# Performance work log

Hardware: AMD Instinct MI355X
Metric: run time of the kernel (lower is better)

Reference implementation:

```python
import jax, jax.numpy as jnp
import numpy as np

B, S, V, D, F, NC = 256, 64, 100000, 64, 10, 10  # batch, seq, vocab, emb_dim, n_feats, n_clusters


def setup_inputs() -> dict:
    key = jax.random.key(0)
    ks = jax.random.split(key, 12)
    ids = jax.random.randint(ks[0], (B, S), 0, V)
    emb_table = jax.random.normal(ks[1], (V, D), dtype=jnp.float32) * 0.02
    comb_w1 = jax.random.normal(ks[2], (2 * D, D), dtype=jnp.float32) / np.sqrt(2 * D)
    comb_b1 = jnp.zeros((D,), jnp.float32)
    comb_w2 = jax.random.normal(ks[3], (D, F), dtype=jnp.float32) / np.sqrt(D)
    comb_b2 = jnp.zeros((F,), jnp.float32)
    freq_w1 = jax.random.normal(ks[4], (D + 1, D), dtype=jnp.float32) / np.sqrt(D + 1)
    freq_b1 = jnp.zeros((D,), jnp.float32)
    freq_w2 = jax.random.normal(ks[5], (D, F), dtype=jnp.float32) / np.sqrt(D)
    freq_b2 = jnp.zeros((F,), jnp.float32)
    cluster_centers = jax.random.normal(ks[6], (NC, D), dtype=jnp.float32)
    cat_freq = jnp.ones((V,), jnp.float32)          # category_frequencies buffer
    total_samples = jnp.array(1.0, jnp.float32)     # total_samples buffer
    return dict(category_ids=ids, emb_table=emb_table,
                comb_w1=comb_w1, comb_b1=comb_b1, comb_w2=comb_w2, comb_b2=comb_b2,
                freq_w1=freq_w1, freq_b1=freq_b1, freq_w2=freq_w2, freq_b2=freq_b2,
                cluster_centers=cluster_centers, cat_freq=cat_freq,
                total_samples=total_samples)


def reference(category_ids, emb_table, comb_w1, comb_b1, comb_w2, comb_b2,
              freq_w1, freq_b1, freq_w2, freq_b2, cluster_centers,
              cat_freq, total_samples):
    emb = emb_table[category_ids]                      # [B,S,D]
    # --- pairwise combination features (vectorized over all i<j pairs) ---
    iu, ju = np.triu_indices(S, 1)                     # P = S*(S-1)/2 pairs
    P = iu.shape[0]
    pairs = jnp.concatenate([emb[:, iu], emb[:, ju]], axis=-1)   # [B,P,2D]
    h = jax.nn.relu(jnp.einsum('bpe,ed->bpd', pairs, comb_w1) + comb_b1)
    combo = jnp.einsum('bpd,df->bpf', h, comb_w2) + comb_b2      # [B,P,F]
    combo_sum = combo.sum(axis=1)                      # [B,F]
    # --- frequency features ---
    freqs = cat_freq[category_ids] / total_samples     # [B,S]
    freq_in = jnp.concatenate([emb, freqs[..., None]], axis=-1)  # [B,S,D+1]
    fh = jax.nn.relu(jnp.einsum('bse,ed->bsd', freq_in, freq_w1) + freq_b1)
    freq_feat = jnp.einsum('bsd,df->bsf', fh, freq_w2) + freq_b2  # [B,S,F]
    # --- cluster assignment features (softmax over -euclidean distances) ---
    d2 = (jnp.sum(emb * emb, axis=-1, keepdims=True)
          + jnp.sum(cluster_centers * cluster_centers, axis=-1)
          - 2.0 * jnp.einsum('bsd,cd->bsc', emb, cluster_centers))
    dist = jnp.sqrt(jnp.maximum(d2, 0.0))              # [B,S,NC]
    cluster_feat = jax.nn.softmax(-dist, axis=-1)      # [B,S,F] (F==NC)
    # --- mean over stacked features: freq + P pair feats (broadcast over seq) + cluster ---
    out = (freq_feat + combo_sum[:, None, :] + cluster_feat) / (P + 2)
    return out
```

## Files before the change

### kernel.cpp

```cpp
#include <hip/hip_runtime.h>
#include <math.h>


typedef _Float16 h2 __attribute__((ext_vector_type(2)));
typedef _Float16 h4 __attribute__((ext_vector_type(4)));
typedef _Float16 h8 __attribute__((ext_vector_type(8)));
union H4u { h4 v; h2 h[2]; };
union H8u { h8 v; h2 h[4]; };

constexpr int BATCH = 256;
constexpr int S = 64, D = 64, F = 10;
constexpr int NPAIR = S * (S - 1) / 2;

constexpr int EMBS = 6144;
constexpr int U2B  = 8448;
constexpr int V2T  = 10496;
constexpr int FHT  = 12608;
constexpr int DI_F = 14784;
constexpr int W2P  = 15488;
constexpr int FRQ  = 15808;
constexpr int PART_F = 0;

__device__ __forceinline__ h2 pk2(float a, float b) {
#if __has_builtin(__builtin_amdgcn_cvt_pkrtz)
  auto t = __builtin_amdgcn_cvt_pkrtz(a, b);
  return __builtin_bit_cast(h2, t);
#else
  h2 r; r.x = (_Float16)a; r.y = (_Float16)b; return r;
#endif
}

__device__ __forceinline__ float fdot2f(h2 a, h2 b, float c) {
#if __has_builtin(__builtin_amdgcn_fdot2)
  typedef __fp16 q2 __attribute__((ext_vector_type(2)));
  return __builtin_amdgcn_fdot2(__builtin_bit_cast(q2, a),
                                __builtin_bit_cast(q2, b), c, false);
#else
  return c + (float)a.x * (float)b.x + (float)a.y * (float)b.y;
#endif
}

__device__ __forceinline__ h2 hmax2z(h2 a) {
#if __has_builtin(__builtin_elementwise_max)
  h2 z = {(_Float16)0, (_Float16)0};
  return __builtin_elementwise_max(a, z);
#else
  h2 r;
  r.x = a.x > (_Float16)0 ? a.x : (_Float16)0;
  r.y = a.y > (_Float16)0 ? a.y : (_Float16)0;
  return r;
#endif
}

__device__ __forceinline__ float lane_up1(float v) {
#if __has_builtin(__builtin_amdgcn_update_dpp)
  int r = __builtin_amdgcn_update_dpp(0, __float_as_int(v), 0xF5, 0xF, 0xF, false);
  return __int_as_float(r);
#else
  return __shfl_down(v, 1, 64);
#endif
}

__global__ __launch_bounds__(1024, 4)
void cat_enc_kernel(const int*   __restrict__ ids,
                    const float* __restrict__ emb_table,
                    const float* __restrict__ comb_w1,
                    const float* __restrict__ comb_b1,
                    const float* __restrict__ comb_w2,
                    const float* __restrict__ comb_b2,
                    const float* __restrict__ freq_w1,
                    const float* __restrict__ freq_b1,
                    const float* __restrict__ freq_w2,
                    const float* __restrict__ freq_b2,
                    const float* __restrict__ centers,
                    const float* __restrict__ cat_freq,
                    const float* __restrict__ total_samples,
                    float*       __restrict__ out)
{
  __shared__ __align__(16) unsigned int ldsu[15872];
  h2*    ldsH = (h2*)ldsu;
  float* ldsf = (float*)ldsu;
  const int tid = threadIdx.x;
  const int b = blockIdx.x, bBase = b * S;
  float ffreg = 0.f;

  {
    int s = tid >> 4, q = tid & 15;
    int id = ids[bBase + s];
    float4 e4 = *(const float4*)(emb_table + (size_t)id * D + q * 4);
    H4u ep; ep.h[0] = pk2(e4.x, e4.y); ep.h[1] = pk2(e4.z, e4.w);
    *(h4*)&ldsH[EMBS + s * 36 + q * 2] = ep.v;
    if (q == 0) ldsf[FRQ + s] = cat_freq[id];

    {
      const int k4 = tid >> 6, dd = tid & 63;
      const float* s0p = comb_w1 + (k4 * 4) * D + dd;
      const float* s1p = s0p + D * D;
      const float* s2p = freq_w1 + (k4 * 4) * D + dd;
      h4* dst = (h4*)ldsu;
      H4u u0; u0.h[0] = pk2(s0p[0], s0p[D]); u0.h[1] = pk2(s0p[2 * D], s0p[3 * D]);
      H4u u1; u1.h[0] = pk2(s1p[0], s1p[D]); u1.h[1] = pk2(s1p[2 * D], s1p[3 * D]);
      H4u u2; u2.h[0] = pk2(s2p[0], s2p[D]); u2.h[1] = pk2(s2p[2 * D], s2p[3 * D]);
      dst[2 * tid]     = u0.v;
      dst[2 * tid + 1] = u1.v;
      dst[2048 + tid]  = u2.v;
    }
    if (tid < 320) {
      int f = tid >> 5, d2 = tid & 31;
      ldsH[W2P + tid] = pk2(freq_w2[(2 * d2) * F + f], freq_w2[(2 * d2 + 1) * F + f]);
    }
  }
  __syncthreads();

  {
    const int wv   = __builtin_amdgcn_readfirstlane((int)(tid >> 6));
    const int lane = tid & 63;
    if (wv < 8) {
      const int d  = lane;
      const int s0 = wv * 8;
      const float invT = 1.0f / total_samples[0];
      const float b1d = comb_b1[d], fb1d = freq_b1[d], fw1L = freq_w1[D * D + d];
      float aU[8], aV[8], aF[8];
#pragma unroll
      for (int si = 0; si < 8; ++si) {
        aU[si] = b1d; aV[si] = 0.f;
        aF[si] = fmaf(ldsf[FRQ + s0 + si] * invT, fw1L, fb1d);
      }
      const h8* WUVp = (const h8*)ldsu;
      const h4* WFp  = (const h4*)(ldsu + 4096);
#pragma unroll 2
      for (int k8 = 0; k8 < 8; ++k8) {
        H8u wa; wa.v = WUVp[(2 * k8) * 64 + d];
        H8u wb; wb.v = WUVp[(2 * k8 + 1) * 64 + d];
        H4u fa; fa.v = WFp[(2 * k8) * 64 + d];
        H4u fb; fb.v = WFp[(2 * k8 + 1) * 64 + d];
#pragma unroll
        for (int si = 0; si < 8; ++si) {
          H8u e; e.v = *(const h8*)&ldsH[EMBS + (s0 + si) * 36 + k8 * 4];
          aU[si] = fdot2f(e.h[0], wa.h[0], aU[si]);
          aU[si] = fdot2f(e.h[1], wa.h[1], aU[si]);
          aV[si] = fdot2f(e.h[0], wa.h[2], aV[si]);
          aV[si] = fdot2f(e.h[1], wa.h[3], aV[si]);
          aF[si] = fdot2f(e.h[0], fa.h[0], aF[si]);
          aF[si] = fdot2f(e.h[1], fa.h[1], aF[si]);
          aU[si] = fdot2f(e.h[2], wb.h[0], aU[si]);
          aU[si] = fdot2f(e.h[3], wb.h[1], aU[si]);
          aV[si] = fdot2f(e.h[2], wb.h[2], aV[si]);
          aV[si] = fdot2f(e.h[3], wb.h[3], aV[si]);
          aF[si] = fdot2f(e.h[2], fb.h[0], aF[si]);
          aF[si] = fdot2f(e.h[3], fb.h[1], aF[si]);
        }
      }
      const bool evenl = ((d & 1) == 0);
      const int d2 = d >> 1;
#pragma unroll
      for (int si = 0; si < 8; ++si) {
        float un = lane_up1(aU[si]);
        float vn = lane_up1(aV[si]);
        float fh = fmaxf(aF[si], 0.f);
        float fn = lane_up1(fh);
        if (evenl) {
          int srow = s0 + si;
          ldsH[U2B + srow * 32 + d2] = pk2(aU[si], un);
          ldsH[V2T + d2 * 66 + srow] = pk2(aV[si], vn);
          ldsH[FHT + srow * 34 + d2] = pk2(fh, fn);
        }
      }
    } else {
      const int s = lane;
      H8u er[8];
#pragma unroll
      for (int k8 = 0; k8 < 8; ++k8)
        er[k8].v = *(const h8*)&ldsH[EMBS + s * 36 + k8 * 4];
      for (int cc = wv - 8; cc < 10; cc += 8) {
        const float* crow = centers + cc * D;
        float acc = 0.f;
#pragma unroll
        for (int k8 = 0; k8 < 8; ++k8) {
#pragma unroll
          for (int t = 0; t < 4; ++t) {
            const int k2 = k8 * 4 + t;
            float t0 = (float)er[k8].h[t].x - crow[2 * k2];
            float t1 = (float)er[k8].h[t].y - crow[2 * k2 + 1];
            acc = fmaf(t0, t0, fmaf(t1, t1, acc));
          }
        }
        ldsf[DI_F + s * 11 + cc] = sqrtf(acc);
      }
    }
  }
  __syncthreads();

  {
    if (tid < 640) {
      int s = tid & 63;
      int f = __builtin_amdgcn_readfirstlane((int)(tid >> 6));
      float acc = freq_b2[f];
      const h8* wrow = (const h8*)&ldsH[W2P + f * 32];
#pragma unroll
      for (int d8 = 0; d8 < 4; ++d8) {
        H8u wf; wf.v = wrow[d8];
        H4u f0; f0.v = *(const h4*)&ldsH[FHT + s * 34 + d8 * 4];
        H4u f1; f1.v = *(const h4*)&ldsH[FHT + s * 34 + d8 * 4 + 2];
        acc = fdot2f(f0.h[0], wf.h[0], acc);
        acc = fdot2f(f0.h[1], wf.h[1], acc);
        acc = fdot2f(f1.h[0], wf.h[2], acc);
        acc = fdot2f(f1.h[1], wf.h[3], acc);
      }
      ffreg = acc;
    }
  }

  {
    const int dg = tid & 31, g = tid >> 5;
    h2 u2a = ldsH[U2B + g * 32 + dg];
    h2 u2b = ldsH[U2B + (63 - g) * 32 + dg];
    h2 za = {(_Float16)0, (_Float16)0};
    h2 acA0 = za, acA1 = za, accb = za;
    const int jsplit = 64 - g;
    int j = g + 1;
    if (j & 1) {
      h2 v2 = ldsH[V2T + dg * 66 + j];
      acA0 = acA0 + hmax2z(u2a + v2);
      ++j;
    }
#pragma unroll 4
    for (; j < 64; j += 2) {
      H4u v; v.v = *(const h4*)&ldsH[V2T + dg * 66 + j];
      acA0 = acA0 + hmax2z(u2a + v.h[0]);
      acA1 = acA1 + hmax2z(u2a + v.h[1]);
      if (j + 1 >= jsplit) {
        if (j >= jsplit) accb = accb + hmax2z(u2b + v.h[0]);
        accb = accb + hmax2z(u2b + v.h[1]);
      }
    }
    h2 at = acA0 + acA1 + accb;
    ldsf[PART_F + g * 64 + 2 * dg]     = (float)at.x;
    ldsf[PART_F + g * 64 + 2 * dg + 1] = (float)at.y;
  }
  __syncthreads();

  if (tid < 640) {
    const int f = __builtin_amdgcn_readfirstlane((int)(tid >> 6));
    const int l = tid & 63;
    float h = 0.f;
#pragma unroll
    for (int g2 = 0; g2 < 32; ++g2) h += ldsf[PART_F + g2 * 64 + l];
    float p = h * comb_w2[l * F + f];
#pragma unroll
    for (int off = 1; off < 64; off <<= 1) p += __shfl_xor(p, off, 64);
    const float cs = fmaf(comb_b2[f], (float)NPAIR, p);
    float dv[10], dmin = 1e30f;
#pragma unroll
    for (int c = 0; c < 10; ++c) { dv[c] = ldsf[DI_F + l * 11 + c]; dmin = fminf(dmin, dv[c]); }
    float sum = 0.f;
#pragma unroll
    for (int c = 0; c < 10; ++c) sum += expf(dmin - dv[c]);
    const float clu = expf(dmin - dv[f]) / sum;
    const float val = (ffreg + cs + clu) * (1.0f / (float)(NPAIR + 2));
    out[(size_t)b * 640 + l * 10 + f] = val;
  }
}

extern "C" void kernel_launch(void* const* d_in, const int* in_sizes, int n_in,
                              void* d_out, int out_size, void* d_ws, size_t ws_size,
                              hipStream_t stream) {
  (void)in_sizes; (void)n_in; (void)d_ws; (void)ws_size; (void)out_size;
  const int*   ids        = (const int*)  d_in[0];
  const float* emb_table  = (const float*)d_in[1];
  const float* comb_w1    = (const float*)d_in[2];
  const float* comb_b1    = (const float*)d_in[3];
  const float* comb_w2    = (const float*)d_in[4];
  const float* comb_b2    = (const float*)d_in[5];
  const float* freq_w1    = (const float*)d_in[6];
  const float* freq_b1    = (const float*)d_in[7];
  const float* freq_w2    = (const float*)d_in[8];
  const float* freq_b2    = (const float*)d_in[9];
  const float* centers    = (const float*)d_in[10];
  const float* cat_freq   = (const float*)d_in[11];
  const float* total_samp = (const float*)d_in[12];
  float* out = (float*)d_out;

  hipLaunchKernelGGL(cat_enc_kernel, dim3(BATCH), dim3(1024), 0, stream,
                     ids, emb_table, comb_w1, comb_b1, comb_w2, comb_b2,
                     freq_w1, freq_b1, freq_w2, freq_b2, centers, cat_freq,
                     total_samp, out);
}
```

Measured before the change: 107.7 us.

## Compute first-layer projections with MFMA 16x16x32 instead of fdot2 loops

Replaces the per-lane fdot2 accumulation for the U, V and frequency first-layer projections with MFMA f16 matrix instructions, using 12 waves (4 row tiles per matrix) instead of 8. The weights are stored transposed in LDS with a padded layout so they can serve as MFMA B operands, and the frequency scaling is folded into the staging step. The cluster-distance work drops from 8 waves to 4 to make room. This is meant to cut VALU time in the projection phase, at the cost of more LDS, a new epilogue layout and less parallelism for the distance computation.

Result: faster. 105.1 us (-2.4%).

```diff
diff --git a/kernel.cpp b/kernel.cpp
--- a/kernel.cpp
+++ b/kernel.cpp
@@ -5,20 +5,23 @@
 typedef _Float16 h2 __attribute__((ext_vector_type(2)));
 typedef _Float16 h4 __attribute__((ext_vector_type(4)));
 typedef _Float16 h8 __attribute__((ext_vector_type(8)));
+typedef float    f4 __attribute__((ext_vector_type(4)));
 union H4u { h4 v; h2 h[2]; };
 union H8u { h8 v; h2 h[4]; };
+union H8q { h8 v; h4 q[2]; };
 
 constexpr int BATCH = 256;
 constexpr int S = 64, D = 64, F = 10;
 constexpr int NPAIR = S * (S - 1) / 2;
 
-constexpr int EMBS = 6144;
-constexpr int U2B  = 8448;
-constexpr int V2T  = 10496;
-constexpr int FHT  = 12608;
-constexpr int DI_F = 14784;
-constexpr int W2P  = 15488;
-constexpr int FRQ  = 15808;
+constexpr int WTMAT = 64 * 34;
+constexpr int EMBS = 6528;
+constexpr int U2B  = 8832;
+constexpr int V2T  = 10880;
+constexpr int FHT  = 12992;
+constexpr int DI_F = 15168;
+constexpr int W2P  = 15872;
+constexpr int FRQ  = 16192;
 constexpr int PART_F = 0;
 
 __device__ __forceinline__ h2 pk2(float a, float b) {
@@ -77,7 +80,7 @@
                     const float* __restrict__ total_samples,
                     float*       __restrict__ out)
 {
-  __shared__ __align__(16) unsigned int ldsu[15872];
+  __shared__ __align__(16) unsigned int ldsu[16256];
   h2*    ldsH = (h2*)ldsu;
   float* ldsf = (float*)ldsu;
   const int tid = threadIdx.x;
@@ -90,20 +93,19 @@
     float4 e4 = *(const float4*)(emb_table + (size_t)id * D + q * 4);
     H4u ep; ep.h[0] = pk2(e4.x, e4.y); ep.h[1] = pk2(e4.z, e4.w);
     *(h4*)&ldsH[EMBS + s * 36 + q * 2] = ep.v;
-    if (q == 0) ldsf[FRQ + s] = cat_freq[id];
-
-    {
-      const int k4 = tid >> 6, dd = tid & 63;
-      const float* s0p = comb_w1 + (k4 * 4) * D + dd;
-      const float* s1p = s0p + D * D;
-      const float* s2p = freq_w1 + (k4 * 4) * D + dd;
-      h4* dst = (h4*)ldsu;
-      H4u u0; u0.h[0] = pk2(s0p[0], s0p[D]); u0.h[1] = pk2(s0p[2 * D], s0p[3 * D]);
-      H4u u1; u1.h[0] = pk2(s1p[0], s1p[D]); u1.h[1] = pk2(s1p[2 * D], s1p[3 * D]);
-      H4u u2; u2.h[0] = pk2(s2p[0], s2p[D]); u2.h[1] = pk2(s2p[2 * D], s2p[3 * D]);
-      dst[2 * tid]     = u0.v;
-      dst[2 * tid + 1] = u1.v;
-      dst[2048 + tid]  = u2.v;
+    if (q == 0) ldsf[FRQ + s] = cat_freq[id] * (1.0f / total_samples[0]);
+
+#pragma unroll
+    for (int it = 0; it < 3; ++it) {
+      const int task = tid + it * 1024;
+      const int m = task >> 10, r = task & 1023;
+      const int d = r & 63, kp = r >> 6;
+      const float* src = ((m == 0) ? comb_w1
+                        : (m == 1) ? comb_w1 + D * D
+                                   : freq_w1) + (4 * kp) * D + d;
+      const float w0 = src[0], w1 = src[D], w2v = src[2 * D], w3 = src[3 * D];
+      H4u wp; wp.h[0] = pk2(w0, w1); wp.h[1] = pk2(w2v, w3);
+      *(h4*)&ldsH[m * WTMAT + d * 34 + 2 * kp] = wp.v;
     }
     if (tid < 320) {
       int f = tid >> 5, d2 = tid & 31;
@@ -115,55 +117,79 @@
   {
     const int wv   = __builtin_amdgcn_readfirstlane((int)(tid >> 6));
     const int lane = tid & 63;
-    if (wv < 8) {
-      const int d  = lane;
-      const int s0 = wv * 8;
-      const float invT = 1.0f / total_samples[0];
-      const float b1d = comb_b1[d], fb1d = freq_b1[d], fw1L = freq_w1[D * D + d];
-      float aU[8], aV[8], aF[8];
-#pragma unroll
-      for (int si = 0; si < 8; ++si) {
-        aU[si] = b1d; aV[si] = 0.f;
-        aF[si] = fmaf(ldsf[FRQ + s0 + si] * invT, fw1L, fb1d);
-      }
-      const h8* WUVp = (const h8*)ldsu;
-      const h4* WFp  = (const h4*)(ldsu + 4096);
-#pragma unroll 2
-      for (int k8 = 0; k8 < 8; ++k8) {
-        H8u wa; wa.v = WUVp[(2 * k8) * 64 + d];
-        H8u wb; wb.v = WUVp[(2 * k8 + 1) * 64 + d];
-        H4u fa; fa.v = WFp[(2 * k8) * 64 + d];
-        H4u fb; fb.v = WFp[(2 * k8 + 1) * 64 + d];
-#pragma unroll
-        for (int si = 0; si < 8; ++si) {
-          H8u e; e.v = *(const h8*)&ldsH[EMBS + (s0 + si) * 36 + k8 * 4];
-          aU[si] = fdot2f(e.h[0], wa.h[0], aU[si]);
-          aU[si] = fdot2f(e.h[1], wa.h[1], aU[si]);
-          aV[si] = fdot2f(e.h[0], wa.h[2], aV[si]);
-          aV[si] = fdot2f(e.h[1], wa.h[3], aV[si]);
-          aF[si] = fdot2f(e.h[0], fa.h[0], aF[si]);
-          aF[si] = fdot2f(e.h[1], fa.h[1], aF[si]);
-          aU[si] = fdot2f(e.h[2], wb.h[0], aU[si]);
-          aU[si] = fdot2f(e.h[3], wb.h[1], aU[si]);
-          aV[si] = fdot2f(e.h[2], wb.h[2], aV[si]);
-          aV[si] = fdot2f(e.h[3], wb.h[3], aV[si]);
-          aF[si] = fdot2f(e.h[2], fb.h[0], aF[si]);
-          aF[si] = fdot2f(e.h[3], fb.h[1], aF[si]);
+    if (wv < 12) {
+      const int mat = wv >> 2, tr = wv & 3;
+      const int col = lane & 15, grp = lane >> 4;
+      const int base = tr * 16 + grp * 4;
+      const int arow = tr * 16 + col;
+      h8 A0 = *(const h8*)&ldsH[EMBS + arow * 36 + grp * 4];
+      h8 A1 = *(const h8*)&ldsH[EMBS + arow * 36 + 16 + grp * 4];
+      const int wtm = mat * WTMAT;
+      f4 acc[4];
+#pragma unroll
+      for (int tc = 0; tc < 4; ++tc) {
+        const int brow = tc * 16 + col;
+        H8q B0, B1;
+        B0.q[0] = *(const h4*)&ldsH[wtm + brow * 34 + grp * 4];
+        B0.q[1] = *(const h4*)&ldsH[wtm + brow * 34 + grp * 4 + 2];
+        B1.q[0] = *(const h4*)&ldsH[wtm + brow * 34 + 16 + grp * 4];
+        B1.q[1] = *(const h4*)&ldsH[wtm + brow * 34 + 16 + grp * 4 + 2];
+        f4 c = {0.f, 0.f, 0.f, 0.f};
+        c = __builtin_amdgcn_mfma_f32_16x16x32_f16(A0, B0.v, c, 0, 0, 0);
+        c = __builtin_amdgcn_mfma_f32_16x16x32_f16(A1, B1.v, c, 0, 0, 0);
+        acc[tc] = c;
+      }
+      const bool evenc = ((col & 1) == 0);
+      if (mat == 0) {
+#pragma unroll
+        for (int tc = 0; tc < 4; ++tc) {
+          const float bv = comb_b1[tc * 16 + col];
+          float v0 = acc[tc][0] + bv, v1 = acc[tc][1] + bv,
+                v2 = acc[tc][2] + bv, v3 = acc[tc][3] + bv;
+          float n0 = lane_up1(v0), n1 = lane_up1(v1),
+                n2 = lane_up1(v2), n3 = lane_up1(v3);
+          if (evenc) {
+            const int d2 = tc * 8 + (col >> 1);
+            ldsH[U2B + (base + 0) * 32 + d2] = pk2(v0, n0);
+            ldsH[U2B + (base + 1) * 32 + d2] = pk2(v1, n1);
+            ldsH[U2B + (base + 2) * 32 + d2] = pk2(v2, n2);
+            ldsH[U2B + (base + 3) * 32 + d2] = pk2(v3, n3);
+          }
         }
-      }
-      const bool evenl = ((d & 1) == 0);
-      const int d2 = d >> 1;
-#pragma unroll
-      for (int si = 0; si < 8; ++si) {
-        float un = lane_up1(aU[si]);
-        float vn = lane_up1(aV[si]);
-        float fh = fmaxf(aF[si], 0.f);
-        float fn = lane_up1(fh);
-        if (evenl) {
-          int srow = s0 + si;
-          ldsH[U2B + srow * 32 + d2] = pk2(aU[si], un);
-          ldsH[V2T + d2 * 66 + srow] = pk2(aV[si], vn);
-          ldsH[FHT + srow * 34 + d2] = pk2(fh, fn);
+      } else if (mat == 1) {
+#pragma unroll
+        for (int tc = 0; tc < 4; ++tc) {
+          float v0 = acc[tc][0], v1 = acc[tc][1],
+                v2 = acc[tc][2], v3 = acc[tc][3];
+          float n0 = lane_up1(v0), n1 = lane_up1(v1),
+                n2 = lane_up1(v2), n3 = lane_up1(v3);
+          if (evenc) {
+            const int d2 = tc * 8 + (col >> 1);
+            H4u w01; w01.h[0] = pk2(v0, n0); w01.h[1] = pk2(v1, n1);
+            *(h4*)&ldsH[V2T + d2 * 66 + base] = w01.v;
+            H4u w23; w23.h[0] = pk2(v2, n2); w23.h[1] = pk2(v3, n3);
+            *(h4*)&ldsH[V2T + d2 * 66 + base + 2] = w23.v;
+          }
+        }
+      } else {
+        const f4 frq4 = *(const f4*)&ldsf[FRQ + base];
+#pragma unroll
+        for (int tc = 0; tc < 4; ++tc) {
+          const int d = tc * 16 + col;
+          const float fwv = freq_w1[D * D + d], fbv = freq_b1[d];
+          float v0 = fmaxf(fmaf(frq4[0], fwv, acc[tc][0]) + fbv, 0.f);
+          float v1 = fmaxf(fmaf(frq4[1], fwv, acc[tc][1]) + fbv, 0.f);
+          float v2 = fmaxf(fmaf(frq4[2], fwv, acc[tc][2]) + fbv, 0.f);
+          float v3 = fmaxf(fmaf(frq4[3], fwv, acc[tc][3]) + fbv, 0.f);
+          float n0 = lane_up1(v0), n1 = lane_up1(v1),
+                n2 = lane_up1(v2), n3 = lane_up1(v3);
+          if (evenc) {
+            const int d2 = tc * 8 + (col >> 1);
+            ldsH[FHT + (base + 0) * 34 + d2] = pk2(v0, n0);
+            ldsH[FHT + (base + 1) * 34 + d2] = pk2(v1, n1);
+            ldsH[FHT + (base + 2) * 34 + d2] = pk2(v2, n2);
+            ldsH[FHT + (base + 3) * 34 + d2] = pk2(v3, n3);
+          }
         }
       }
     } else {
@@ -172,7 +198,7 @@
 #pragma unroll
       for (int k8 = 0; k8 < 8; ++k8)
         er[k8].v = *(const h8*)&ldsH[EMBS + s * 36 + k8 * 4];
-      for (int cc = wv - 8; cc < 10; cc += 8) {
+      for (int cc = wv - 12; cc < 10; cc += 4) {
         const float* crow = centers + cc * D;
         float acc = 0.f;
 #pragma unroll
```
